# Kernel optimization log

Hardware: AMD Instinct MI355X
Metric: run time of the kernel (lower is better)

The kernel has to match this reference:

```python
import jax, jax.numpy as jnp
import numpy as np

N = 2048; E = 5; C = 2; W_IN = 256; W_OUT = 128; NUM_CLASS = 8; NT = 1024


def _norm(H, add):
    # faithful to GTN.norm: transpose, zero diagonal, (optionally add I),
    # row-degree-normalize (diag(deg^-1) @ H expressed as row scaling), transpose back
    Ht = H.T
    n = Ht.shape[0]
    eye = jnp.eye(n, dtype=Ht.dtype)
    Ht = Ht * (1.0 - eye)
    if add:
        Ht = Ht + eye
    deg = jnp.sum(Ht, axis=1)
    deg_inv = jnp.where(deg == 0, jnp.zeros_like(deg), 1.0 / deg)
    return (deg_inv[:, None] * Ht).T


def _gtconv(A_e, w):
    # A_e: [E, N, N]; w: [C, E]; softmax over edge types then weighted sum
    return jnp.einsum('ce,enm->cnm', jax.nn.softmax(w, axis=1), A_e)


def setup_inputs() -> dict:
    key = jax.random.key(0)
    ks = jax.random.split(key, 12)
    A = jax.random.uniform(ks[0], (N, N, E), dtype=jnp.float32)
    X = jax.random.uniform(ks[1], (N, W_IN), dtype=jnp.float32)  # BCE target, in [0,1]
    target_x = jax.random.randint(ks[2], (NT,), 0, N)
    target = jax.random.randint(ks[3], (NT,), 0, NUM_CLASS)
    w0a = 0.1 * jax.random.normal(ks[4], (C, E), dtype=jnp.float32)
    w0b = 0.1 * jax.random.normal(ks[5], (C, E), dtype=jnp.float32)
    w1a = 0.1 * jax.random.normal(ks[6], (C, E), dtype=jnp.float32)
    W = jax.random.normal(ks[7], (W_IN, W_OUT), dtype=jnp.float32) * (1.0 / np.sqrt(W_IN))
    W1 = jax.random.normal(ks[8], (W_OUT * C, W_OUT), dtype=jnp.float32) * (1.0 / np.sqrt(W_OUT * C))
    W2 = jax.random.normal(ks[9], (W_OUT * C, W_IN), dtype=jnp.float32) * (1.0 / np.sqrt(W_OUT * C))
    lin_w = jax.random.normal(ks[10], (NUM_CLASS, W_OUT), dtype=jnp.float32) * (1.0 / np.sqrt(W_OUT))
    lin_b = jnp.zeros((NUM_CLASS,), dtype=jnp.float32)
    return {"A": A, "X": X, "W": W, "W1": W1, "W2": W2, "lin_w": lin_w,
            "lin_b": lin_b, "w0a": w0a, "w0b": w0b, "w1a": w1a,
            "target_x": target_x, "target": target}


def reference(A, X, W, W1, W2, lin_w, lin_b, w0a, w0b, w1a, target_x, target):
    A_e = jnp.transpose(A, (2, 0, 1))          # [E, N, N]
    # layer 0 (first=True): H = conv1(A) @ conv2(A)
    a = _gtconv(A_e, w0a)                      # [C, N, N]
    b = _gtconv(A_e, w0b)
    H = jnp.einsum('cij,cjk->cik', a, b)
    # layer 1 (first=False): H = normalization(H) @ conv1(A)
    Hn = jax.vmap(lambda h: _norm(h, False))(H)
    a1 = _gtconv(A_e, w1a)
    H = jnp.einsum('cij,cjk->cik', Hn, a1)
    # per-channel GCN conv: relu(norm(H_c, add=True).T @ (X @ W)), concat on features
    XW = X @ W                                 # [N, w_out]
    Hn2 = jax.vmap(lambda h: _norm(h, True))(H)
    Xc = jax.nn.relu(jnp.einsum('cji,jd->cid', Hn2, XW))  # [C, N, w_out]
    n = X.shape[0]
    X_cat = jnp.transpose(Xc, (1, 0, 2)).reshape(n, -1)   # [N, C*w_out]
    # sum channels, then the two head GCN convs share norm(H_sum, add=True)
    Hs = _norm(jnp.sum(H, axis=0), True)
    X_r = Hs.T @ (X_cat @ W2)                  # [N, w_in]
    X_o = Hs.T @ (X_cat @ W1)                  # [N, w_out]
    y = X_o[target_x] @ lin_w.T + lin_b        # [NT, num_class]
    # clamp reconstruction into [0,1] via sigmoid on out-of-range entries
    X_r = jnp.where(X_r > 1, jax.nn.sigmoid(X_r), X_r)
    X_r = jnp.where(X_r < 0, jax.nn.sigmoid(X_r), X_r)
    p = jnp.clip(X_r, 1e-7, 1.0 - 1e-7)
    lossR = -jnp.mean(X * jnp.log(p) + (1.0 - X) * jnp.log1p(-p))
    logp = jax.nn.log_softmax(y, axis=-1)
    lossC = -jnp.mean(jnp.take_along_axis(logp, target[:, None], axis=1))
    loss = lossC + lossR
    Ws = (jax.lax.stop_gradient(jax.nn.softmax(w0a, axis=1)),
          jax.lax.stop_gradient(jax.nn.softmax(w0b, axis=1)),
          jax.lax.stop_gradient(jax.nn.softmax(w1a, axis=1)))
    return (loss, y, Ws, lossR)
```

## Files before the change

### kernel.cpp

```cpp
#include <hip/hip_runtime.h>
#include <hip/hip_bf16.h>
#include <math.h>

#define NDIM 2048
#define EDIM 5
#define CDIM 2
#define WIN 256
#define WOUT 128
#define NCLS 8
#define NTGT 1024
#define NN ((size_t)NDIM * NDIM)
#define HNSC 256.0f
#define HNSCI 0.00390625f

typedef __attribute__((ext_vector_type(8))) short short8v;
typedef __attribute__((ext_vector_type(4))) float float4v;
typedef __attribute__((ext_vector_type(8))) int int8v;
typedef __attribute__((ext_vector_type(4))) int int4v;
typedef __attribute__((ext_vector_type(2))) int int2v;

__device__ __forceinline__ void gl2lds16(const void* g, void* l) {
  __builtin_amdgcn_global_load_lds((__attribute__((address_space(1))) const unsigned int*)g,
                                   (__attribute__((address_space(3))) unsigned int*)l, 16, 0, 0);
}
__device__ __forceinline__ float bf2f(unsigned short u) {
  return __uint_as_float(((unsigned)u) << 16);
}
__device__ __forceinline__ unsigned short f2bf(float f) {
  __hip_bfloat16 h = __float2bfloat16(f);
  return *(unsigned short*)&h;
}
__device__ __forceinline__ unsigned int pk4fp8(float a, float b, float c, float d) {
  int w = __builtin_amdgcn_cvt_pk_fp8_f32(a, b, 0, false);
  return (unsigned int)__builtin_amdgcn_cvt_pk_fp8_f32(c, d, w, true);
}

#define N_XBF (NDIM * WIN)
#define N_WT (WIN * WOUT)
#define N_W12T (384 * WIN)
#define N_PREP (N_XBF + N_WT + N_W12T + CDIM * NDIM + 16 + 30)
__global__ __launch_bounds__(256) void wsum_mega_k(
    const float* __restrict__ A, const float* __restrict__ w0a,
    const float* __restrict__ w0b, const float* __restrict__ w1a,
    unsigned char* __restrict__ a_out, unsigned char* __restrict__ bT,
    unsigned char* __restrict__ a1T,
    float* __restrict__ acc, float* __restrict__ deg,
    const float* __restrict__ X, const float* __restrict__ W,
    const float* __restrict__ W1, const float* __restrict__ W2,
    __hip_bfloat16* __restrict__ Xbf, __hip_bfloat16* __restrict__ WTbf,
    __hip_bfloat16* __restrict__ W12Tbf,
    float* __restrict__ dout) {
  const int b = blockIdx.x;
  const int tid = threadIdx.x;
  if (b >= 4096) {
    int idx = (b - 4096) * 256 + tid;
    if (idx < N_XBF) { Xbf[idx] = __float2bfloat16(X[idx]); return; }
    idx -= N_XBF;
    if (idx < N_WT) {
      int d = idx >> 8, k = idx & 255;
      WTbf[idx] = __float2bfloat16(W[k * WOUT + d]);
      return;
    }
    idx -= N_WT;
    if (idx < N_W12T) {
      int j = idx >> 8, k = idx & 255;
      W12Tbf[idx] = __float2bfloat16(j < 128 ? W1[k * 128 + j] : W2[k * 256 + (j - 128)]);
      return;
    }
    idx -= N_W12T;
    if (idx < CDIM * NDIM) { deg[idx] = 0.f; return; }
    idx -= CDIM * NDIM;
    if (idx < 16) { acc[idx] = 0.f; return; }
    idx -= 16;
    if (idx < 30) {
      int m = idx / 10, rr = idx - m * 10, c = rr / 5, e = rr - c * 5;
      const float* src = (m == 0) ? w0a : (m == 1) ? w0b : w1a;
      float mx = -1e30f;
      for (int t = 0; t < 5; ++t) mx = fmaxf(mx, src[c * 5 + t]);
      float s = 0.f, ve = 0.f;
      for (int t = 0; t < 5; ++t) {
        float ex = expf(src[c * 5 + t] - mx);
        s += ex;
        if (t == e) ve = ex;
      }
      dout[1 + NTGT * NCLS + idx] = ve / s;
    }
    return;
  }
  __shared__ float swl[32];
  __shared__ float tb[CDIM][32][33];
  __shared__ float tc[CDIM][32][33];
  if (tid < 6) {
    int m = tid >> 1, c = tid & 1;
    const float* src = (m == 0) ? w0a : (m == 1) ? w0b : w1a;
    float mx = -1e30f;
    for (int e = 0; e < 5; ++e) mx = fmaxf(mx, src[c * 5 + e]);
    float ex[5]; float s = 0.f;
    for (int e = 0; e < 5; ++e) { ex[e] = expf(src[c * 5 + e] - mx); s += ex[e]; }
    for (int e = 0; e < 5; ++e) swl[m * 10 + c * 5 + e] = ex[e] / s;
  }
  __syncthreads();
  const int bx = (b & 63) * 32, by = (b >> 6) * 32;
  const int tx4 = tid & 7, ty = tid >> 3;
  const int n = by + ty, m0 = bx + tx4 * 4;
  const float* ap = A + ((size_t)n * NDIM + m0) * EDIM;
  float4 f0 = *(const float4*)(ap);
  float4 f1 = *(const float4*)(ap + 4);
  float4 f2 = *(const float4*)(ap + 8);
  float4 f3 = *(const float4*)(ap + 12);
  float4 f4 = *(const float4*)(ap + 16);
  float v[4][5] = {{f0.x, f0.y, f0.z, f0.w, f1.x},
                   {f1.y, f1.z, f1.w, f2.x, f2.y},
                   {f2.z, f2.w, f3.x, f3.y, f3.z},
                   {f3.w, f4.x, f4.y, f4.z, f4.w}};
#pragma unroll
  for (int c = 0; c < CDIM; ++c) {
    float sa[4], sb[4], sc[4];
#pragma unroll
    for (int t = 0; t < 4; ++t) {
      sa[t] = swl[c*5]*v[t][0] + swl[c*5+1]*v[t][1] + swl[c*5+2]*v[t][2] +
              swl[c*5+3]*v[t][3] + swl[c*5+4]*v[t][4];
      sb[t] = swl[10+c*5]*v[t][0] + swl[10+c*5+1]*v[t][1] + swl[10+c*5+2]*v[t][2] +
              swl[10+c*5+3]*v[t][3] + swl[10+c*5+4]*v[t][4];
      sc[t] = swl[20+c*5]*v[t][0] + swl[20+c*5+1]*v[t][1] + swl[20+c*5+2]*v[t][2] +
              swl[20+c*5+3]*v[t][3] + swl[20+c*5+4]*v[t][4];
      tb[c][ty][tx4 * 4 + t] = sb[t];
      tc[c][ty][tx4 * 4 + t] = sc[t];
    }
    *(unsigned int*)(a_out + c * NN + (size_t)n * NDIM + m0) =
        pk4fp8(sa[0], sa[1], sa[2], sa[3]);
  }
  __syncthreads();
  const int mm = bx + ty, nn0 = by + tx4 * 4;
#pragma unroll
  for (int c = 0; c < CDIM; ++c) {
    float b0 = tb[c][tx4*4+0][ty], b1 = tb[c][tx4*4+1][ty];
    float b2 = tb[c][tx4*4+2][ty], b3 = tb[c][tx4*4+3][ty];
    float c0 = tc[c][tx4*4+0][ty], c1 = tc[c][tx4*4+1][ty];
    float c2 = tc[c][tx4*4+2][ty], c3 = tc[c][tx4*4+3][ty];
    *(unsigned int*)(bT + c * NN + (size_t)mm * NDIM + nn0) = pk4fp8(b0, b1, b2, b3);
    *(unsigned int*)(a1T + c * NN + (size_t)mm * NDIM + nn0) = pk4fp8(c0, c1, c2, c3);
  }
}

__device__ __forceinline__ void fp8_gemm_body(
    const unsigned char* __restrict__ A, const unsigned char* __restrict__ B,
    __hip_bfloat16* __restrict__ Cp, float* __restrict__ csp,
    int K, int ldc, int row0, int col0,
    unsigned char* As, unsigned char* Bs) {
  const int tid = threadIdx.x;
  const int lane = tid & 63;
  const int wave = tid >> 6;
  const int wr = (wave >> 1) * 64;
  const int wc = (wave & 1) * 64;
  const int q = lane >> 4;
  const int r = lane & 15;

  float4v acc[4][4] = {};

  const int srow = lane >> 3;
  const int scol = ((lane & 7) ^ (srow & 7)) * 16;
  const int fsw = r & 15 & 7;

  for (int k0 = 0; k0 < K; k0 += 128) {
    __syncthreads();
#pragma unroll
    for (int s = 0; s < 4; ++s) {
      gl2lds16(A + (size_t)(row0 + s * 32 + wave * 8 + srow) * K + k0 + scol,
               As + s * 4096 + wave * 1024);
      gl2lds16(B + (size_t)(col0 + s * 32 + wave * 8 + srow) * K + k0 + scol,
               Bs + s * 4096 + wave * 1024);
    }
    __syncthreads();

    union { int8v v; int4v h[2]; } ua[4], ub[4];
#pragma unroll
    for (int i = 0; i < 4; ++i) {
      const unsigned char* pa = As + (size_t)(wr + i * 16 + r) * 128;
      const unsigned char* pb = Bs + (size_t)(wc + i * 16 + r) * 128;
      ua[i].h[0] = *(const int4v*)(pa + (((2 * q) ^ fsw) * 16));
      ua[i].h[1] = *(const int4v*)(pa + (((2 * q + 1) ^ fsw) * 16));
      ub[i].h[0] = *(const int4v*)(pb + (((2 * q) ^ fsw) * 16));
      ub[i].h[1] = *(const int4v*)(pb + (((2 * q + 1) ^ fsw) * 16));
    }
#pragma unroll
    for (int i = 0; i < 4; ++i)
#pragma unroll
      for (int j = 0; j < 4; ++j)
        acc[i][j] = __builtin_amdgcn_mfma_scale_f32_16x16x128_f8f6f4(
            ua[i].v, ub[j].v, acc[i][j], 0, 0, 0, 0x7F7F7F7F, 0, 0x7F7F7F7F);
  }

#pragma unroll
  for (int i = 0; i < 4; ++i) {
    int row = row0 + wr + i * 16 + q * 4;
#pragma unroll
    for (int j = 0; j < 4; ++j) {
      int col = col0 + wc + j * 16 + r;
#pragma unroll
      for (int e = 0; e < 4; ++e)
        Cp[(size_t)(row + e) * ldc + col] = __float2bfloat16(acc[i][j][e]);
    }
  }

  if (csp) {
#pragma unroll
    for (int j = 0; j < 4; ++j) {
      int col = col0 + wc + j * 16 + r;
      float s = 0.f;
#pragma unroll
      for (int i = 0; i < 4; ++i) {
        int rowb = row0 + wr + i * 16 + q * 4;
#pragma unroll
        for (int e = 0; e < 4; ++e)
          if (rowb + e != col) s += acc[i][j][e];
      }
      s += __shfl_xor(s, 16, 64);
      s += __shfl_xor(s, 32, 64);
      if (lane < 16) atomicAdd(&csp[col], s);
    }
  }
}

__device__ __forceinline__ void bf16_gemm_body(
    const __hip_bfloat16* __restrict__ A, const __hip_bfloat16* __restrict__ B,
    __hip_bfloat16* __restrict__ Cp, int K, int ldc, int row0, int col0,
    int kbeg, int kend, char* As, char* Bs) {
  const int tid = threadIdx.x;
  const int lane = tid & 63;
  const int wave = tid >> 6;
  const int wr = (wave >> 1) * 64;
  const int wc = (wave & 1) * 64;
  const int q = lane >> 4;
  const int r = lane & 15;

  float4v acc[4][4] = {};

  const int srow = lane >> 3;
  const int scol = ((lane & 7) ^ (srow & 7)) * 8;
  const int fsw = r & 7;

  for (int k0 = kbeg; k0 < kend; k0 += 64) {
    __syncthreads();
#pragma unroll
    for (int s = 0; s < 4; ++s) {
      gl2lds16(A + (size_t)(row0 + s * 32 + wave * 8 + srow) * K + k0 + scol,
               As + s * 4096 + wave * 1024);
      gl2lds16(B + (size_t)(col0 + s * 32 + wave * 8 + srow) * K + k0 + scol,
               Bs + s * 4096 + wave * 1024);
    }
    __syncthreads();
#pragma unroll
    for (int h = 0; h < 2; ++h) {
      short8v af[4], bf[4];
#pragma unroll
      for (int i = 0; i < 4; ++i) {
        af[i] = *(const short8v*)(As + (size_t)(wr + i * 16 + r) * 128 +
                                  (((h * 4 + q) ^ fsw) * 16));
        bf[i] = *(const short8v*)(Bs + (size_t)(wc + i * 16 + r) * 128 +
                                  (((h * 4 + q) ^ fsw) * 16));
      }
#pragma unroll
      for (int i = 0; i < 4; ++i)
#pragma unroll
        for (int j = 0; j < 4; ++j)
          acc[i][j] = __builtin_amdgcn_mfma_f32_16x16x32_bf16(af[i], bf[j], acc[i][j], 0, 0, 0);
    }
  }

#pragma unroll
  for (int i = 0; i < 4; ++i) {
    int row = row0 + wr + i * 16 + q * 4;
#pragma unroll
    for (int j = 0; j < 4; ++j) {
      int col = col0 + wc + j * 16 + r;
#pragma unroll
      for (int e = 0; e < 4; ++e)
        Cp[(size_t)(row + e) * ldc + col] = __float2bfloat16(acc[i][j][e]);
    }
  }
}

__global__ __launch_bounds__(256) void gemm1_xwt_k(
    const unsigned char* __restrict__ P_a, const unsigned char* __restrict__ P_bT,
    __hip_bfloat16* __restrict__ H_bf, float* __restrict__ deg,
    const __hip_bfloat16* __restrict__ WTbf, const __hip_bfloat16* __restrict__ Xbf,
    __hip_bfloat16* __restrict__ XWT) {
  __shared__ __align__(16) unsigned char smem[32768];
  const int z = blockIdx.z;
  if (z < 2) {
    fp8_gemm_body(P_a + (size_t)z * NN, P_bT + (size_t)z * NN,
                  H_bf + (size_t)z * NN, deg + (size_t)z * NDIM,
                  NDIM, NDIM, blockIdx.y * 128, blockIdx.x * 128,
                  smem, smem + 16384);
  } else {
    if (blockIdx.y != 0) return;
    bf16_gemm_body(WTbf, Xbf, XWT, WIN, NDIM, 0, blockIdx.x * 128,
                   0, WIN, (char*)smem, (char*)smem + 16384);
  }
}

__global__ __launch_bounds__(256) void gemm2_k(
    const unsigned char* __restrict__ P_a1T, const unsigned char* __restrict__ P_Hn,
    __hip_bfloat16* __restrict__ H1T_bf) {
  __shared__ __align__(16) unsigned char smem[32768];
  const int z = blockIdx.z;
  fp8_gemm_body(P_a1T + (size_t)z * NN, P_Hn + (size_t)z * NN,
                H1T_bf + (size_t)z * NN, nullptr,
                NDIM, NDIM, blockIdx.y * 128, blockIdx.x * 128,
                smem, smem + 16384);
}

__global__ __launch_bounds__(256) void mfma_bt_k(
    const __hip_bfloat16* __restrict__ Ab, const __hip_bfloat16* __restrict__ Bt,
    __hip_bfloat16* __restrict__ Cv, int K, int ldc,
    size_t sA, size_t sB, size_t sC, size_t sSplit, int nsplit) {
  __shared__ __align__(16) char smem[32768];
  const int batch = blockIdx.z / nsplit;
  const int split = blockIdx.z - batch * nsplit;
  const int kchunk = K / nsplit;
  bf16_gemm_body(Ab + (size_t)batch * sA, Bt + (size_t)batch * sB,
                 Cv + (size_t)batch * sC + (size_t)split * sSplit,
                 K, ldc, blockIdx.y * 128, blockIdx.x * 128,
                 split * kchunk, split * kchunk + kchunk,
                 smem, smem + 16384);
}

__global__ __launch_bounds__(256) void col_scale_k(const __hip_bfloat16* __restrict__ H,
                                                   const float* __restrict__ deg,
                                                   unsigned char* __restrict__ out) {
  size_t base = ((size_t)blockIdx.x * 256 + threadIdx.x) * 8;
  int c = (int)(base >> 22);
  int i = (int)((base >> 11) & (NDIM - 1));
  int j0 = (int)(base & (NDIM - 1));
  union { short8v v; unsigned short u[8]; } p;
  p.v = *(const short8v*)(H + base);
  float f[8];
#pragma unroll
  for (int t = 0; t < 8; ++t) {
    int j = j0 + t;
    float d = deg[c * NDIM + j];
    float inv = (d == 0.f) ? 0.f : HNSC / d;
    float v = (i == j) ? 0.f : bf2f(p.u[t]);
    f[t] = v * inv;
  }
  int2v o;
  o.x = (int)pk4fp8(f[0], f[1], f[2], f[3]);
  o.y = (int)pk4fp8(f[4], f[5], f[6], f[7]);
  *(int2v*)(out + base) = o;
}

__global__ __launch_bounds__(256) void rowmega_k(const __hip_bfloat16* __restrict__ H1T,
                                                 __hip_bfloat16* __restrict__ Hn2T,
                                                 __hip_bfloat16* __restrict__ HsT) {
  const int m = blockIdx.x;
  const int tid = threadIdx.x;
  const size_t rb = (size_t)m * NDIM + tid * 8;
  union { short8v v; unsigned short u[8]; } a0, a1;
  a0.v = *(const short8v*)(H1T + rb);
  a1.v = *(const short8v*)(H1T + NN + rb);
  float v0[8], v1[8];
  float s0 = 0.f, s1 = 0.f;
#pragma unroll
  for (int t = 0; t < 8; ++t) {
    v0[t] = bf2f(a0.u[t]) * HNSCI;
    v1[t] = bf2f(a1.u[t]) * HNSCI;
    s0 += v0[t]; s1 += v1[t];
  }
  __shared__ float ds[2];
  __shared__ float red[2][4];
  __shared__ float bc[3];
  if (tid == (m >> 3)) { ds[0] = v0[m & 7]; ds[1] = v1[m & 7]; }
  for (int off = 32; off > 0; off >>= 1) {
    s0 += __shfl_down(s0, off, 64);
    s1 += __shfl_down(s1, off, 64);
  }
  if ((tid & 63) == 0) { red[0][tid >> 6] = s0; red[1][tid >> 6] = s1; }
  __syncthreads();
  if (tid == 0) {
    float t0 = red[0][0] + red[0][1] + red[0][2] + red[0][3];
    float t1 = red[1][0] + red[1][1] + red[1][2] + red[1][3];
    float r0 = t0 - ds[0] + 1.f;
    float r1 = t1 - ds[1] + 1.f;
    float rs = t0 + t1 - ds[0] - ds[1] + 1.f;
    bc[0] = (r0 == 0.f) ? 0.f : 1.f / r0;
    bc[1] = (r1 == 0.f) ? 0.f : 1.f / r1;
    bc[2] = (rs == 0.f) ? 0.f : 1.f / rs;
  }
  __syncthreads();
  float i0 = bc[0], i1 = bc[1], is = bc[2];
  union { short8v v; unsigned short u[8]; } o0, o1, os;
#pragma unroll
  for (int t = 0; t < 8; ++t) {
    bool dg = (tid * 8 + t == m);
    o0.u[t] = f2bf((dg ? 1.f : v0[t]) * i0);
    o1.u[t] = f2bf((dg ? 1.f : v1[t]) * i1);
    os.u[t] = f2bf((dg ? 1.f : (v0[t] + v1[t])) * is);
  }
  *(short8v*)(Hn2T + rb) = o0.v;
  *(short8v*)(Hn2T + NN + rb) = o1.v;
  *(short8v*)(HsT + rb) = os.v;
}

__global__ __launch_bounds__(256) void reduce_relu_k(const __hip_bfloat16* __restrict__ P7,
                                                     __hip_bfloat16* __restrict__ Xcat) {
  int idx = blockIdx.x * 256 + threadIdx.x;
  int c = idx >> 18;
  int rem = idx & 262143;
  float s = 0.f;
#pragma unroll
  for (int sp = 0; sp < 8; ++sp)
    s += __bfloat162float(P7[(size_t)c * 2097152 + (size_t)sp * 262144 + rem]);
  int n = rem >> 7, d = rem & 127;
  Xcat[(size_t)n * 256 + (c << 7) + d] = __float2bfloat16(fmaxf(s, 0.f));
}

__global__ __launch_bounds__(256) void loss_mega_k(const __hip_bfloat16* __restrict__ P10,
                                                   const float* __restrict__ X,
                                                   const float* __restrict__ lin_w,
                                                   const float* __restrict__ lin_b,
                                                   const int* __restrict__ txs,
                                                   const int* __restrict__ tgt,
                                                   float* __restrict__ yout,
                                                   float* __restrict__ acc) {
  const int b = blockIdx.x;
  const int tid = threadIdx.x;
  if (b < 2048) {
    float xr = 0.f;
#pragma unroll
    for (int sp = 0; sp < 8; ++sp)
      xr += __bfloat162float(P10[(size_t)sp * 786432 + (size_t)b * 384 + 128 + tid]);
    if (xr > 1.f) xr = 1.f / (1.f + expf(-xr));
    if (xr < 0.f) xr = 1.f / (1.f + expf(-xr));
    float p = fminf(fmaxf(xr, 1e-7f), 1.f - 1e-7f);
    float xv = X[(size_t)b * WIN + tid];
    float t = xv * logf(p) + (1.f - xv) * log1pf(-p);
    for (int off = 32; off > 0; off >>= 1) t += __shfl_down(t, off, 64);
    __shared__ float red[4];
    if ((tid & 63) == 0) red[tid >> 6] = t;
    __syncthreads();
    if (tid == 0) atomicAdd(acc + 1, red[0] + red[1] + red[2] + red[3]);
    return;
  }
  const int t = b - 2048;
  __shared__ float xo[WOUT];
  __shared__ float ys[NCLS];
  int x = txs[t];
  if (tid < WOUT) {
    float s = 0.f;
#pragma unroll
    for (int sp = 0; sp < 8; ++sp)
      s += __bfloat162float(P10[(size_t)sp * 786432 + (size_t)x * 384 + tid]);
    xo[tid] = s;
  }
  __syncthreads();
  if (tid < NCLS) {
    float s = lin_b[tid];
    for (int d = 0; d < WOUT; ++d) s += xo[d] * lin_w[tid * WOUT + d];
    ys[tid] = s;
    yout[(size_t)t * NCLS + tid] = s;
  }
  __syncthreads();
  if (tid == 0) {
    float m = ys[0];
    for (int k = 1; k < NCLS; ++k) m = fmaxf(m, ys[k]);
    float se = 0.f;
    for (int k = 0; k < NCLS; ++k) se += expf(ys[k] - m);
    float lse = m + logf(se);
    atomicAdd(acc, lse - ys[tgt[t]]);
  }
}

__global__ void finalize_k(const float* __restrict__ acc, float* __restrict__ dout) {
  float lossC = acc[0] / (float)NTGT;
  float lossR = -acc[1] / (float)(NDIM * WIN);
  dout[0] = lossC + lossR;
  dout[1 + NTGT * NCLS + 30] = lossR;
}

extern "C" void kernel_launch(void* const* d_in, const int* in_sizes, int n_in,
                              void* d_out, int out_size, void* d_ws, size_t ws_size,
                              hipStream_t stream) {
  const float* A    = (const float*)d_in[0];
  const float* X    = (const float*)d_in[1];
  const float* W    = (const float*)d_in[2];
  const float* W1   = (const float*)d_in[3];
  const float* W2   = (const float*)d_in[4];
  const float* linw = (const float*)d_in[5];
  const float* linb = (const float*)d_in[6];
  const float* w0a  = (const float*)d_in[7];
  const float* w0b  = (const float*)d_in[8];
  const float* w1a  = (const float*)d_in[9];
  const int* txs    = (const int*)d_in[10];
  const int* tgt    = (const int*)d_in[11];
  float* dout = (float*)d_out;

  float* ws = (float*)d_ws;
  unsigned char* wb = (unsigned char*)d_ws;
  unsigned char* P_a   = wb;
  unsigned char* P_bT  = wb + 2 * NN;
  unsigned char* P_a1T = wb + 4 * NN;
  unsigned char* P_Hn  = wb + 6 * NN;
  __hip_bfloat16* H_bf   = (__hip_bfloat16*)(ws + 2 * NN);
  __hip_bfloat16* H1T_bf = (__hip_bfloat16*)(ws + 3 * NN);
  __hip_bfloat16* Hn2T   = (__hip_bfloat16*)(ws + 4 * NN);
  __hip_bfloat16* HsT    = (__hip_bfloat16*)(ws);
  float* sm   = ws + 5 * NN;
  float* acc   = sm;                 sm += 16;
  float* deg   = sm;                 sm += CDIM * NDIM;
  __hip_bfloat16* Xbf    = (__hip_bfloat16*)sm;  sm += N_XBF / 2;
  __hip_bfloat16* WTbf   = (__hip_bfloat16*)sm;  sm += N_WT / 2;
  __hip_bfloat16* W12Tbf = (__hip_bfloat16*)sm;  sm += N_W12T / 2;
  __hip_bfloat16* XWT    = (__hip_bfloat16*)sm;  sm += (size_t)WOUT * NDIM / 2;
  __hip_bfloat16* Xcat   = (__hip_bfloat16*)sm;  sm += (size_t)NDIM * 256 / 2;
  __hip_bfloat16* XC12T  = (__hip_bfloat16*)sm;  sm += (size_t)384 * NDIM / 2;
  __hip_bfloat16* P7bf   = (__hip_bfloat16*)sm;  sm += (size_t)16 * 262144 / 2;
  __hip_bfloat16* P10bf  = (__hip_bfloat16*)sm;  sm += (size_t)8 * 786432 / 2;

  dim3 blk256(256);

  wsum_mega_k<<<dim3(4096 + (N_PREP + 255) / 256), blk256, 0, stream>>>(
      A, w0a, w0b, w1a, P_a, P_bT, P_a1T, acc, deg, X, W, W1, W2,
      Xbf, WTbf, W12Tbf, dout);
  gemm1_xwt_k<<<dim3(16, 16, 3), blk256, 0, stream>>>(P_a, P_bT, H_bf, deg,
                                                      WTbf, Xbf, XWT);
  col_scale_k<<<dim3((unsigned)(2 * NN / 2048)), blk256, 0, stream>>>(H_bf, deg, P_Hn);
  gemm2_k<<<dim3(16, 16, 2), blk256, 0, stream>>>(P_a1T, P_Hn, H1T_bf);
  rowmega_k<<<dim3(NDIM), blk256, 0, stream>>>(H1T_bf, Hn2T, HsT);
  mfma_bt_k<<<dim3(1, 16, 16), blk256, 0, stream>>>(Hn2T, XWT, P7bf, NDIM, WOUT,
                                                    NN, 0, 2097152, 262144, 8);
  reduce_relu_k<<<dim3(2048), blk256, 0, stream>>>(P7bf, Xcat);
  mfma_bt_k<<<dim3(16, 3, 1), blk256, 0, stream>>>(W12Tbf, Xcat, XC12T, 256, NDIM,
                                                   0, 0, 0, 0, 1);
  mfma_bt_k<<<dim3(3, 16, 8), blk256, 0, stream>>>(HsT, XC12T, P10bf, NDIM, 384,
                                                   0, 0, 0, 786432, 8);
  loss_mega_k<<<dim3(2048 + NTGT), blk256, 0, stream>>>(P10bf, X, linw, linb, txs, tgt,
                                                        dout + 1, acc);
  finalize_k<<<dim3(1), dim3(1), 0, stream>>>(acc, dout);
}
```

Baseline: 289.3 us.

## Split K in half for both FP8 adjacency GEMMs and sum partials downstream

Both FP8 N×N GEMMs now split the K dimension into two halves, doubling the grid to give the GPU more independent tiles. Each half writes its own bf16 partial product. `col_scale_k` and `rowmega_k` read both partials and add them before normalising. This raises parallelism and occupancy for the large GEMMs. The cost is extra HBM traffic for writing and rereading the second partial buffer, plus rounding each partial to bf16 before the sum.

```diff
diff --git a/kernel.cpp b/kernel.cpp
--- a/kernel.cpp
+++ b/kernel.cpp
@@ -146,7 +146,7 @@
 __device__ __forceinline__ void fp8_gemm_body(
     const unsigned char* __restrict__ A, const unsigned char* __restrict__ B,
     __hip_bfloat16* __restrict__ Cp, float* __restrict__ csp,
-    int K, int ldc, int row0, int col0,
+    int K, int ldc, int row0, int col0, int kbeg, int kend,
     unsigned char* As, unsigned char* Bs) {
   const int tid = threadIdx.x;
   const int lane = tid & 63;
@@ -160,9 +160,9 @@
 
   const int srow = lane >> 3;
   const int scol = ((lane & 7) ^ (srow & 7)) * 16;
-  const int fsw = r & 15 & 7;
-
-  for (int k0 = 0; k0 < K; k0 += 128) {
+  const int fsw = r & 7;
+
+  for (int k0 = kbeg; k0 < kend; k0 += 128) {
     __syncthreads();
 #pragma unroll
     for (int s = 0; s < 4; ++s) {
@@ -283,16 +283,17 @@
 
 __global__ __launch_bounds__(256) void gemm1_xwt_k(
     const unsigned char* __restrict__ P_a, const unsigned char* __restrict__ P_bT,
-    __hip_bfloat16* __restrict__ H_bf, float* __restrict__ deg,
+    __hip_bfloat16* __restrict__ Hp, float* __restrict__ deg,
     const __hip_bfloat16* __restrict__ WTbf, const __hip_bfloat16* __restrict__ Xbf,
     __hip_bfloat16* __restrict__ XWT) {
   __shared__ __align__(16) unsigned char smem[32768];
   const int z = blockIdx.z;
-  if (z < 2) {
-    fp8_gemm_body(P_a + (size_t)z * NN, P_bT + (size_t)z * NN,
-                  H_bf + (size_t)z * NN, deg + (size_t)z * NDIM,
+  if (z < 4) {
+    const int c = z >> 1, s = z & 1;
+    fp8_gemm_body(P_a + (size_t)c * NN, P_bT + (size_t)c * NN,
+                  Hp + (size_t)s * 2 * NN + (size_t)c * NN, deg + (size_t)c * NDIM,
                   NDIM, NDIM, blockIdx.y * 128, blockIdx.x * 128,
-                  smem, smem + 16384);
+                  s * 1024, s * 1024 + 1024, smem, smem + 16384);
   } else {
     if (blockIdx.y != 0) return;
     bf16_gemm_body(WTbf, Xbf, XWT, WIN, NDIM, 0, blockIdx.x * 128,
@@ -302,13 +303,14 @@
 
 __global__ __launch_bounds__(256) void gemm2_k(
     const unsigned char* __restrict__ P_a1T, const unsigned char* __restrict__ P_Hn,
-    __hip_bfloat16* __restrict__ H1T_bf) {
+    __hip_bfloat16* __restrict__ Qp) {
   __shared__ __align__(16) unsigned char smem[32768];
   const int z = blockIdx.z;
-  fp8_gemm_body(P_a1T + (size_t)z * NN, P_Hn + (size_t)z * NN,
-                H1T_bf + (size_t)z * NN, nullptr,
+  const int c = z >> 1, s = z & 1;
+  fp8_gemm_body(P_a1T + (size_t)c * NN, P_Hn + (size_t)c * NN,
+                Qp + (size_t)s * 2 * NN + (size_t)c * NN, nullptr,
                 NDIM, NDIM, blockIdx.y * 128, blockIdx.x * 128,
-                smem, smem + 16384);
+                s * 1024, s * 1024 + 1024, smem, smem + 16384);
 }
 
 __global__ __launch_bounds__(256) void mfma_bt_k(
@@ -326,22 +328,23 @@
                  smem, smem + 16384);
 }
 
-__global__ __launch_bounds__(256) void col_scale_k(const __hip_bfloat16* __restrict__ H,
+__global__ __launch_bounds__(256) void col_scale_k(const __hip_bfloat16* __restrict__ Hp,
                                                    const float* __restrict__ deg,
                                                    unsigned char* __restrict__ out) {
   size_t base = ((size_t)blockIdx.x * 256 + threadIdx.x) * 8;
   int c = (int)(base >> 22);
   int i = (int)((base >> 11) & (NDIM - 1));
   int j0 = (int)(base & (NDIM - 1));
-  union { short8v v; unsigned short u[8]; } p;
-  p.v = *(const short8v*)(H + base);
+  union { short8v v; unsigned short u[8]; } p0, p1;
+  p0.v = *(const short8v*)(Hp + base);
+  p1.v = *(const short8v*)(Hp + 2 * NN + base);
   float f[8];
 #pragma unroll
   for (int t = 0; t < 8; ++t) {
     int j = j0 + t;
     float d = deg[c * NDIM + j];
     float inv = (d == 0.f) ? 0.f : HNSC / d;
-    float v = (i == j) ? 0.f : bf2f(p.u[t]);
+    float v = (i == j) ? 0.f : (bf2f(p0.u[t]) + bf2f(p1.u[t]));
     f[t] = v * inv;
   }
   int2v o;
@@ -350,21 +353,23 @@
   *(int2v*)(out + base) = o;
 }
 
-__global__ __launch_bounds__(256) void rowmega_k(const __hip_bfloat16* __restrict__ H1T,
+__global__ __launch_bounds__(256) void rowmega_k(const __hip_bfloat16* __restrict__ Qp,
                                                  __hip_bfloat16* __restrict__ Hn2T,
                                                  __hip_bfloat16* __restrict__ HsT) {
   const int m = blockIdx.x;
   const int tid = threadIdx.x;
   const size_t rb = (size_t)m * NDIM + tid * 8;
-  union { short8v v; unsigned short u[8]; } a0, a1;
-  a0.v = *(const short8v*)(H1T + rb);
-  a1.v = *(const short8v*)(H1T + NN + rb);
+  union { short8v v; unsigned short u[8]; } a0, b0, a1, b1;
+  a0.v = *(const short8v*)(Qp + rb);
+  b0.v = *(const short8v*)(Qp + 2 * NN + rb);
+  a1.v = *(const short8v*)(Qp + NN + rb);
+  b1.v = *(const short8v*)(Qp + 3 * NN + rb);
   float v0[8], v1[8];
   float s0 = 0.f, s1 = 0.f;
 #pragma unroll
   for (int t = 0; t < 8; ++t) {
-    v0[t] = bf2f(a0.u[t]) * HNSCI;
-    v1[t] = bf2f(a1.u[t]) * HNSCI;
+    v0[t] = (bf2f(a0.u[t]) + bf2f(b0.u[t])) * HNSCI;
+    v1[t] = (bf2f(a1.u[t]) + bf2f(b1.u[t])) * HNSCI;
     s0 += v0[t]; s1 += v1[t];
   }
   __shared__ float ds[2];
@@ -501,10 +506,10 @@
   unsigned char* P_bT  = wb + 2 * NN;
   unsigned char* P_a1T = wb + 4 * NN;
   unsigned char* P_Hn  = wb + 6 * NN;
-  __hip_bfloat16* H_bf   = (__hip_bfloat16*)(ws + 2 * NN);
-  __hip_bfloat16* H1T_bf = (__hip_bfloat16*)(ws + 3 * NN);
-  __hip_bfloat16* Hn2T   = (__hip_bfloat16*)(ws + 4 * NN);
-  __hip_bfloat16* HsT    = (__hip_bfloat16*)(ws);
+  __hip_bfloat16* Hp   = (__hip_bfloat16*)(ws + 2 * NN);
+  __hip_bfloat16* Qp   = Hp;
+  __hip_bfloat16* Hn2T = (__hip_bfloat16*)(ws + 4 * NN);
+  __hip_bfloat16* HsT  = (__hip_bfloat16*)(ws);
   float* sm   = ws + 5 * NN;
   float* acc   = sm;                 sm += 16;
   float* deg   = sm;                 sm += CDIM * NDIM;
@@ -522,11 +527,11 @@
   wsum_mega_k<<<dim3(4096 + (N_PREP + 255) / 256), blk256, 0, stream>>>(
       A, w0a, w0b, w1a, P_a, P_bT, P_a1T, acc, deg, X, W, W1, W2,
       Xbf, WTbf, W12Tbf, dout);
-  gemm1_xwt_k<<<dim3(16, 16, 3), blk256, 0, stream>>>(P_a, P_bT, H_bf, deg,
+  gemm1_xwt_k<<<dim3(16, 16, 5), blk256, 0, stream>>>(P_a, P_bT, Hp, deg,
                                                       WTbf, Xbf, XWT);
-  col_scale_k<<<dim3((unsigned)(2 * NN / 2048)), blk256, 0, stream>>>(H_bf, deg, P_Hn);
-  gemm2_k<<<dim3(16, 16, 2), blk256, 0, stream>>>(P_a1T, P_Hn, H1T_bf);
-  rowmega_k<<<dim3(NDIM), blk256, 0, stream>>>(H1T_bf, Hn2T, HsT);
+  col_scale_k<<<dim3((unsigned)(2 * NN / 2048)), blk256, 0, stream>>>(Hp, deg, P_Hn);
+  gemm2_k<<<dim3(16, 16, 4), blk256, 0, stream>>>(P_a1T, P_Hn, Qp);
+  rowmega_k<<<dim3(NDIM), blk256, 0, stream>>>(Qp, Hn2T, HsT);
   mfma_bt_k<<<dim3(1, 16, 16), blk256, 0, stream>>>(Hn2T, XWT, P7bf, NDIM, WOUT,
                                                     NN, 0, 2097152, 262144, 8);
   reduce_relu_k<<<dim3(2048), blk256, 0, stream>>>(P7bf, Xcat);
```

Measured after the change: 310.5 us. 1.07x slower.
